# Kernel tuning notes

Measured on AMD Instinct MI355X. Metric: run time of the kernel, lower is better.

The kernel has to match this reference:

```python
import jax, jax.numpy as jnp
import numpy as np

N, D, H, F, T = 2048, 256, 4, 64, 64
HF = H * F


def setup_inputs() -> dict:
    key = jax.random.key(0)
    ks = jax.random.split(key, 24)
    f32 = jnp.float32
    emb = jax.random.normal(ks[0], (N, D), f32)
    y_as_x = jax.random.normal(ks[1], (N, T), f32)
    adj = (jax.random.uniform(ks[2], (N, N)) < 0.02).astype(f32)
    u = lambda k, shape, s: jax.random.uniform(k, shape, f32, -s, s)
    stdv = 1.0 / np.sqrt(HF)
    inp = dict(emb=emb, y_as_x=y_as_x, adj=adj)
    for i, p in enumerate(['pos', 'neg']):
        o = 3 + i * 6
        inp[p + '_w'] = u(ks[o], (D, HF), stdv)
        inp[p + '_wu'] = u(ks[o + 1], (H, F), 1.0)
        inp[p + '_wv'] = u(ks[o + 2], (H, F), 1.0)
        inp[p + '_b'] = u(ks[o + 3], (1, HF), stdv)
        inp[p + '_pw'] = u(ks[o + 4], (D, HF), 0.02)
        inp[p + '_pb'] = jnp.zeros((HF,), f32)
    inp['self_w'] = u(ks[15], (D, D), 0.02)
    inp['self_b'] = jnp.zeros((D,), f32)
    inp['mlp_pos_w'] = u(ks[16], (HF, D), 0.02)
    inp['mlp_pos_b'] = jnp.zeros((D,), f32)
    inp['mlp_neg_w'] = u(ks[17], (HF, D), 0.02)
    inp['mlp_neg_b'] = jnp.zeros((D,), f32)
    inp['sem_w1'] = u(ks[18], (D, D), 0.02)
    inp['sem_b1'] = jnp.zeros((D,), f32)
    inp['sem_w2'] = u(ks[19], (D, 1), 0.02)
    return inp


def _gat(x, mask, w, wu, wv, b, pw, pb):
    # x: [N,D], mask: [N,N] bool; multi-head GAT with dense masked softmax
    s = (x @ w).reshape(N, H, F).transpose(1, 0, 2)          # [H,N,F]
    f1 = jnp.einsum('hnf,hf->hn', s, wu)                     # u-score per node
    f2 = jnp.einsum('hnf,hf->hn', s, wv)                     # v-score per node
    logits = f1[:, None, :] + f2[:, :, None]                 # [H,N,N], i<-j
    logits = jax.nn.leaky_relu(logits, 0.2)
    masked = jnp.where(mask[None], logits, -1e9)
    attn = jnp.where(mask[None], jax.nn.softmax(masked, axis=2), 0.0)
    out = jnp.einsum('hij,hjf->hif', attn, s)                # [H,N,F]
    out = out.transpose(1, 0, 2).reshape(N, HF) + b
    return out + x @ pw + pb


def reference(emb, y_as_x, adj, pos_w, pos_wu, pos_wv, pos_b, pos_pw, pos_pb,
              neg_w, neg_wu, neg_wv, neg_b, neg_pw, neg_pb,
              self_w, self_b, mlp_pos_w, mlp_pos_b, mlp_neg_w, mlp_neg_b,
              sem_w1, sem_b1, sem_w2):
    # batched pairwise correlation (replaces the per-node Python loop)
    yc = y_as_x - y_as_x.mean(axis=1, keepdims=True)         # centered
    dot = yc @ yc.T                                          # [N,N]
    std = jnp.sqrt((yc ** 2).sum(axis=1) / (T - 1))          # torch std: ddof=1
    corr = dot / (std[:, None] * std[None, :])
    edge = adj != 0
    pos_mask = edge & (corr >= 0.1)
    neg_mask = edge & (corr < 0.1)

    pos_sup = _gat(emb, pos_mask, pos_w, pos_wu, pos_wv, pos_b, pos_pw, pos_pb)
    neg_sup = _gat(emb, neg_mask, neg_w, neg_wu, neg_wv, neg_b, neg_pw, neg_pb)

    sup = emb @ self_w + self_b
    pos_sup = pos_sup @ mlp_pos_w + mlp_pos_b
    neg_sup = neg_sup @ mlp_neg_w + mlp_neg_b

    all_emb = jnp.stack((sup, pos_sup, neg_sup), axis=1)     # [N,3,D]
    # semantic attention over the 3 relation channels
    wlog = jnp.tanh(all_emb @ sem_w1 + sem_b1) @ sem_w2      # [N,3,1]
    beta = jax.nn.softmax(wlog, axis=1)
    x = (beta * all_emb).sum(axis=1)                         # [N,D]
    # PairNorm PN-SI
    x = x - x.mean(axis=0)
    rownorm = jnp.sqrt(1e-6 + (x ** 2).sum(axis=1, keepdims=True))
    return x / rownorm
```

## Files before the change

kernel.cpp:

```cpp
#include <hip/hip_runtime.h>
#include <hip/hip_bf16.h>

#define KN  2048
#define KD  256
#define KH  4
#define KF  64
#define KT  64
#define NCS 32

typedef __attribute__((ext_vector_type(8))) short short8;
typedef __attribute__((ext_vector_type(4))) float floatx4;

__device__ __forceinline__ float wave_sum(float v) {
    #pragma unroll
    for (int o = 32; o > 0; o >>= 1) v += __shfl_xor(v, o, 64);
    return v;
}
__device__ __forceinline__ float wave_max(float v) {
    #pragma unroll
    for (int o = 32; o > 0; o >>= 1) v = fmaxf(v, __shfl_xor(v, o, 64));
    return v;
}
__device__ __forceinline__ short f2bs(float x) {
    union { __hip_bfloat16 h; short s; } u;
    u.h = __float2bfloat16(x);
    return u.s;
}

__global__ __launch_bounds__(256) void setup_kernel(const float* __restrict__ y,
                                                    float* __restrict__ ycs) {
    int w = threadIdx.x >> 6, lane = threadIdx.x & 63;
    int n = blockIdx.x * 4 + w;
    float v = y[n * KT + lane];
    float mean = wave_sum(v) * (1.0f / KT);
    float yc = v - mean;
    float ss = wave_sum(yc * yc);
    ycs[n * KT + lane] = yc * rsqrtf(ss * (1.0f / (KT - 1)));
}

__device__ __forceinline__ void corr_body(const float* __restrict__ ycs,
                                          const float* __restrict__ adj,
                                          unsigned char* __restrict__ code,
                                          int blk, char* smem) {
    float (*As)[68] = (float(*)[68])smem;
    float (*Bs)[68] = (float(*)[68])(smem + 4352);
    int bi = 0, rem = blk;
    while (rem >= 32 - bi) { rem -= 32 - bi; bi++; }
    int bj = bi + rem;
    int i0 = bi * 64, j0 = bj * 64;
    int t = threadIdx.x;
    int tx = t & 15, ty = t >> 4;
    int ar = t >> 2, ac = (t & 3) * 4;
    float acc[4][4] = {};
    for (int kt = 0; kt < KT; kt += 16) {
        float4 a4 = *reinterpret_cast<const float4*>(&ycs[(size_t)(i0 + ar) * KT + kt + ac]);
        float4 b4 = *reinterpret_cast<const float4*>(&ycs[(size_t)(j0 + ar) * KT + kt + ac]);
        As[ac + 0][ar] = a4.x; As[ac + 1][ar] = a4.y; As[ac + 2][ar] = a4.z; As[ac + 3][ar] = a4.w;
        Bs[ac + 0][ar] = b4.x; Bs[ac + 1][ar] = b4.y; Bs[ac + 2][ar] = b4.z; Bs[ac + 3][ar] = b4.w;
        __syncthreads();
        #pragma unroll
        for (int kk = 0; kk < 16; kk++) {
            float4 av = *reinterpret_cast<const float4*>(&As[kk][ty * 4]);
            float4 bv = *reinterpret_cast<const float4*>(&Bs[kk][tx * 4]);
            float a4v[4] = {av.x, av.y, av.z, av.w};
            float b4v[4] = {bv.x, bv.y, bv.z, bv.w};
            #pragma unroll
            for (int ii = 0; ii < 4; ii++)
                #pragma unroll
                for (int jj = 0; jj < 4; jj++) acc[ii][jj] += a4v[ii] * b4v[jj];
        }
        __syncthreads();
    }
    #pragma unroll
    for (int ii = 0; ii < 4; ii++) {
        int i = i0 + ty * 4 + ii;
        int jb = j0 + tx * 4;
        float4 av4 = *reinterpret_cast<const float4*>(&adj[(size_t)i * KN + jb]);
        float a4v[4] = {av4.x, av4.y, av4.z, av4.w};
        uchar4 cc;
        unsigned char* c = (unsigned char*)&cc;
        #pragma unroll
        for (int jj = 0; jj < 4; jj++)
            c[jj] = (a4v[jj] != 0.0f) ? ((acc[ii][jj] >= 0.1f) ? 1 : 2) : 0;
        *reinterpret_cast<uchar4*>(&code[(size_t)i * KN + jb]) = cc;
    }
    if (bi != bj) {
        #pragma unroll
        for (int jj = 0; jj < 4; jj++) {
            int j = j0 + tx * 4 + jj;
            int ib = i0 + ty * 4;
            float4 av4 = *reinterpret_cast<const float4*>(&adj[(size_t)j * KN + ib]);
            float a4v[4] = {av4.x, av4.y, av4.z, av4.w};
            uchar4 cc;
            unsigned char* c = (unsigned char*)&cc;
            #pragma unroll
            for (int ii = 0; ii < 4; ii++)
                c[ii] = (a4v[ii] != 0.0f) ? ((acc[ii][jj] >= 0.1f) ? 1 : 2) : 0;
            *reinterpret_cast<uchar4*>(&code[(size_t)j * KN + ib]) = cc;
        }
    }
}

template <bool TANH>
__device__ __forceinline__ void mfma_gemm_body(
    const float* __restrict__ A, int lda, int bm,
    const float* __restrict__ B, int ldb, int bn,
    const float* __restrict__ bias,
    float* __restrict__ C, int ldc, int cn,
    float* __restrict__ f1h, float* __restrict__ f2h,
    const float* __restrict__ wu_h, const float* __restrict__ wv_h,
    char* smem)
{
    short* As = (short*)smem;
    short* Bs = (short*)(smem + 5120);
    int t = threadIdx.x;
    int w = t >> 6, lane = t & 63;
    int m16 = lane & 15, kq = lane >> 4;
    floatx4 acc0 = {0,0,0,0}, acc1 = {0,0,0,0}, acc2 = {0,0,0,0}, acc3 = {0,0,0,0};
    int ar = t >> 2, acq = (t & 3) * 8;
    int bnn = t & 63, bkg = (t >> 6) * 8;
    for (int kt = 0; kt < KD; kt += 32) {
        const float* pa = &A[(size_t)(bm + ar) * lda + kt + acq];
        float4 a0 = *(const float4*)pa;
        float4 a1 = *(const float4*)(pa + 4);
        short8 av;
        av[0] = f2bs(a0.x); av[1] = f2bs(a0.y); av[2] = f2bs(a0.z); av[3] = f2bs(a0.w);
        av[4] = f2bs(a1.x); av[5] = f2bs(a1.y); av[6] = f2bs(a1.z); av[7] = f2bs(a1.w);
        const float* pb = &B[(size_t)(kt + bkg) * ldb + bn + bnn];
        short8 bv;
        #pragma unroll
        for (int u = 0; u < 8; u++) bv[u] = f2bs(pb[(size_t)u * ldb]);
        __syncthreads();
        *(short8*)&As[ar * 40 + acq] = av;
        *(short8*)&Bs[bnn * 40 + bkg] = bv;
        __syncthreads();
        short8 af  = *(short8*)&As[(w * 16 + m16) * 40 + kq * 8];
        short8 bf0 = *(short8*)&Bs[( 0 + m16) * 40 + kq * 8];
        short8 bf1 = *(short8*)&Bs[(16 + m16) * 40 + kq * 8];
        short8 bf2 = *(short8*)&Bs[(32 + m16) * 40 + kq * 8];
        short8 bf3 = *(short8*)&Bs[(48 + m16) * 40 + kq * 8];
        acc0 = __builtin_amdgcn_mfma_f32_16x16x32_bf16(af, bf0, acc0, 0, 0, 0);
        acc1 = __builtin_amdgcn_mfma_f32_16x16x32_bf16(af, bf1, acc1, 0, 0, 0);
        acc2 = __builtin_amdgcn_mfma_f32_16x16x32_bf16(af, bf2, acc2, 0, 0, 0);
        acc3 = __builtin_amdgcn_mfma_f32_16x16x32_bf16(af, bf3, acc3, 0, 0, 0);
    }
    int row0 = bm + w * 16 + kq * 4;
    floatx4 accs[4] = {acc0, acc1, acc2, acc3};
    #pragma unroll
    for (int nb = 0; nb < 4; nb++) {
        #pragma unroll
        for (int r = 0; r < 4; r++) {
            int col = nb * 16 + m16;
            float v = accs[nb][r] + (bias ? bias[col] : 0.0f);
            if (TANH) {
                float vc = fminf(fmaxf(v, -9.0f), 9.0f);
                float ex = __expf(2.0f * vc);
                v = (ex - 1.0f) / (ex + 1.0f);
            }
            C[(size_t)(row0 + r) * ldc + cn + col] = v;
        }
    }
    if (f1h) {
        float wuv[4], wvv[4];
        #pragma unroll
        for (int nb = 0; nb < 4; nb++) { wuv[nb] = wu_h[nb * 16 + m16]; wvv[nb] = wv_h[nb * 16 + m16]; }
        #pragma unroll
        for (int r = 0; r < 4; r++) {
            float p1 = accs[0][r] * wuv[0] + accs[1][r] * wuv[1] + accs[2][r] * wuv[2] + accs[3][r] * wuv[3];
            float p2 = accs[0][r] * wvv[0] + accs[1][r] * wvv[1] + accs[2][r] * wvv[2] + accs[3][r] * wvv[3];
            #pragma unroll
            for (int o = 1; o < 16; o <<= 1) {
                p1 += __shfl_xor(p1, o, 64);
                p2 += __shfl_xor(p2, o, 64);
            }
            if (m16 == 0) { f1h[row0 + r] = p1; f2h[row0 + r] = p2; }
        }
    }
}

struct EmbPtrs {
    float *S_pos, *S_neg, *P_pos, *P_neg, *sup;
    float *f1p, *f2p, *f1n, *f2n;
};
__global__ __launch_bounds__(256, 4) void phase1_kernel(
    const float* __restrict__ ycs, const float* __restrict__ adj,
    unsigned char* __restrict__ code,
    const float* __restrict__ emb,
    const float* __restrict__ pos_w, const float* __restrict__ neg_w,
    const float* __restrict__ pos_pw, const float* __restrict__ neg_pw,
    const float* __restrict__ self_w,
    const float* __restrict__ pos_pb, const float* __restrict__ neg_pb,
    const float* __restrict__ self_b,
    const float* __restrict__ pos_wu, const float* __restrict__ pos_wv,
    const float* __restrict__ neg_wu, const float* __restrict__ neg_wv,
    float* __restrict__ colsum, EmbPtrs ep)
{
    __shared__ alignas(16) char smem[10240];
    int blk = blockIdx.x;
    if (blk < 528) {
        corr_body(ycs, adj, code, blk, smem);
        return;
    }
    if (blk >= 1168) {
        for (int j = threadIdx.x; j < NCS * KD; j += 256) colsum[j] = 0.0f;
        return;
    }
    int b = blk - 528;
    int tn = b % 20, tm = b / 20;
    int buf = tn >> 2, coloff = (tn & 3) * 64;
    int h = tn & 3;
    const float* B; const float* bias; float* C;
    float *f1h = nullptr, *f2h = nullptr;
    const float *wu_h = nullptr, *wv_h = nullptr;
    if (buf == 0) {
        B = pos_w;  bias = nullptr; C = ep.S_pos;
        f1h = ep.f1p + h * KN; f2h = ep.f2p + h * KN;
        wu_h = pos_wu + h * KF; wv_h = pos_wv + h * KF;
    } else if (buf == 1) {
        B = neg_w;  bias = nullptr; C = ep.S_neg;
        f1h = ep.f1n + h * KN; f2h = ep.f2n + h * KN;
        wu_h = neg_wu + h * KF; wv_h = neg_wv + h * KF;
    } else if (buf == 2) { B = pos_pw; bias = pos_pb + coloff;  C = ep.P_pos; }
    else if (buf == 3)   { B = neg_pw; bias = neg_pb + coloff;  C = ep.P_neg; }
    else                 { B = self_w; bias = self_b + coloff;  C = ep.sup; }
    mfma_gemm_body<false>(emb, KD, tm * 64, B, KD, coloff, bias,
                          C, KD, coloff, f1h, f2h, wu_h, wv_h, smem);
}

__global__ __launch_bounds__(256, 4) void gemm_mlp(const float* __restrict__ Astack,
                                                   const float* __restrict__ B0,
                                                   const float* __restrict__ B1,
                                                   const float* __restrict__ b0,
                                                   const float* __restrict__ b1,
                                                   float* __restrict__ Cstack,
                                                   const float* __restrict__ sup,
                                                   const float* __restrict__ semw1,
                                                   const float* __restrict__ semb1,
                                                   float* __restrict__ T0) {
    __shared__ alignas(16) char smem[10240];
    int by = blockIdx.y;
    int cn = blockIdx.x * 64;
    if (by < 64) {
        int bm = by * 64;
        bool sel = bm >= KN;
        mfma_gemm_body<false>(Astack, KD, bm, sel ? B1 : B0, KD, cn,
                              (sel ? b1 : b0) + cn, Cstack, KD, cn,
                              nullptr, nullptr, nullptr, nullptr, smem);
    } else {
        int bm = (by - 64) * 64;
        mfma_gemm_body<true>(sup, KD, bm, semw1, KD, cn,
                             semb1 + cn, T0, KD, cn,
                             nullptr, nullptr, nullptr, nullptr, smem);
    }
}

__global__ __launch_bounds__(256, 4) void gemm_sem(const float* __restrict__ Astack,
                                                   const float* __restrict__ B,
                                                   const float* __restrict__ bias,
                                                   float* __restrict__ Cstack) {
    __shared__ alignas(16) char smem[10240];
    int cn = blockIdx.x * 64;
    mfma_gemm_body<true>(Astack, KD, blockIdx.y * 64, B, KD, cn,
                         bias + cn, Cstack, KD, cn,
                         nullptr, nullptr, nullptr, nullptr, smem);
}

#define MAXE 256
__global__ __launch_bounds__(256) void attn_kernel(
    const unsigned char* __restrict__ code,
    const float* __restrict__ f1p, const float* __restrict__ f2p,
    const float* __restrict__ Sp, const float* __restrict__ Pp,
    const float* __restrict__ bp, float* __restrict__ Gp,
    const float* __restrict__ f1n, const float* __restrict__ f2n,
    const float* __restrict__ Sn, const float* __restrict__ Pn,
    const float* __restrict__ bn_, float* __restrict__ Gn)
{
    __shared__ alignas(16) int jl[MAXE];
    __shared__ alignas(16) float lg[KH][MAXE];
    __shared__ int cnt;
    int blk = blockIdx.x;
    int rel = blk >> 11;
    int i = blk & (KN - 1);
    unsigned char want = rel ? (unsigned char)2 : (unsigned char)1;
    const float* f1 = rel ? f1n : f1p;
    const float* f2 = rel ? f2n : f2p;
    const float* S  = rel ? Sn : Sp;
    const float* P  = rel ? Pn : Pp;
    const float* b  = rel ? bn_ : bp;
    float* G        = rel ? Gn : Gp;
    int w = threadIdx.x >> 6, lane = threadIdx.x & 63;
    if (threadIdx.x == 0) cnt = 0;
    __syncthreads();
    #pragma unroll
    for (int it = 0; it < 2; it++) {
        int base = w * 512 + it * 256;
        uchar4 cv = *reinterpret_cast<const uchar4*>(&code[(size_t)i * KN + base + lane * 4]);
        const unsigned char* ce = (const unsigned char*)&cv;
        #pragma unroll
        for (int e = 0; e < 4; e++) {
            bool p = (ce[e] == want);
            unsigned long long bal = __ballot(p);
            int tot = __popcll(bal);
            int basepos = 0;
            if (lane == 0 && tot) basepos = atomicAdd(&cnt, tot);
            basepos = __shfl(basepos, 0, 64);
            if (p) {
                int idx = basepos + __popcll(bal & ((1ull << lane) - 1ull));
                if (idx < MAXE) jl[idx] = base + lane * 4 + e;
            }
        }
    }
    __syncthreads();
    int count = cnt; if (count > MAXE) count = MAXE;
    int countR = (count + 3) & ~3;
    if (threadIdx.x < countR - count) jl[count + threadIdx.x] = 0;
    __syncthreads();
    int h = w;
    float f2i = f2[h * KN + i];
    float m = -1e30f;
    for (int k = lane; k < count; k += 64) {
        int j = jl[k];
        float x = f1[h * KN + j] + f2i;
        x = (x > 0.0f) ? x : 0.2f * x;
        lg[h][k] = x;
        m = fmaxf(m, x);
    }
    m = wave_max(m);
    float ps = 0.0f;
    for (int k = lane; k < count; k += 64) {
        float e = __expf(lg[h][k] - m);
        lg[h][k] = e;
        ps += e;
    }
    float denom = wave_sum(ps);
    for (int k2 = count + lane; k2 < countR; k2 += 64) lg[h][k2] = 0.0f;
    int g = lane >> 4, q4 = (lane & 15) * 4;
    const float* Sh4 = S + h * KF + q4;
    float ax = 0.0f, ay = 0.0f, az = 0.0f, aw = 0.0f;
    for (int k = 0; k < countR; k += 4) {
        int j = jl[k + g];
        float wgt = lg[h][k + g];
        float4 sv = *reinterpret_cast<const float4*>(&Sh4[(size_t)j * KD]);
        ax += wgt * sv.x; ay += wgt * sv.y; az += wgt * sv.z; aw += wgt * sv.w;
    }
    #pragma unroll
    for (int o = 16; o < 64; o <<= 1) {
        ax += __shfl_xor(ax, o, 64); ay += __shfl_xor(ay, o, 64);
        az += __shfl_xor(az, o, 64); aw += __shfl_xor(aw, o, 64);
    }
    if (g == 0) {
        float inv = count ? (1.0f / denom) : 0.0f;
        int col = h * KF + q4;
        size_t idx = (size_t)i * KD + col;
        float4 pv = *reinterpret_cast<const float4*>(&P[idx]);
        float4 o4;
        o4.x = ax * inv + b[col + 0] + pv.x;
        o4.y = ay * inv + b[col + 1] + pv.y;
        o4.z = az * inv + b[col + 2] + pv.z;
        o4.w = aw * inv + b[col + 3] + pv.w;
        *reinterpret_cast<float4*>(&G[idx]) = o4;
    }
}

__global__ __launch_bounds__(256) void combine_kernel(const float* __restrict__ T0,
                                                      const float* __restrict__ T1,
                                                      const float* __restrict__ T2,
                                                      const float* __restrict__ w2,
                                                      const float* __restrict__ sup,
                                                      const float* __restrict__ psup,
                                                      const float* __restrict__ nsup,
                                                      float* __restrict__ X,
                                                      float* __restrict__ colsum) {
    int n = blockIdx.x, d = threadIdx.x;
    size_t idx = (size_t)n * KD + d;
    float w2d = w2[d];
    float p0 = T0[idx] * w2d, p1 = T1[idx] * w2d, p2 = T2[idx] * w2d;
    __shared__ float sbuf[4][3];
    int wv = d >> 6, lane = d & 63;
    float s0 = wave_sum(p0), s1 = wave_sum(p1), s2 = wave_sum(p2);
    if (lane == 0) { sbuf[wv][0] = s0; sbuf[wv][1] = s1; sbuf[wv][2] = s2; }
    __syncthreads();
    float w0 = sbuf[0][0] + sbuf[1][0] + sbuf[2][0] + sbuf[3][0];
    float w1 = sbuf[0][1] + sbuf[1][1] + sbuf[2][1] + sbuf[3][1];
    float w2l = sbuf[0][2] + sbuf[1][2] + sbuf[2][2] + sbuf[3][2];
    float mm = fmaxf(w0, fmaxf(w1, w2l));
    float e0 = __expf(w0 - mm), e1 = __expf(w1 - mm), e2 = __expf(w2l - mm);
    float inv = 1.0f / (e0 + e1 + e2);
    float x = (e0 * inv) * sup[idx] + (e1 * inv) * psup[idx] + (e2 * inv) * nsup[idx];
    X[idx] = x;
    atomicAdd(&colsum[(n & (NCS - 1)) * KD + d], x);
}

__global__ __launch_bounds__(256) void final_kernel(const float* __restrict__ X,
                                                    const float* __restrict__ colsum,
                                                    float* __restrict__ out) {
    int n = blockIdx.x, d = threadIdx.x;
    float cs = 0.0f;
    #pragma unroll
    for (int r = 0; r < NCS; r++) cs += colsum[r * KD + d];
    float mean = cs * (1.0f / KN);
    float xc = X[(size_t)n * KD + d] - mean;
    __shared__ float sbuf[4];
    int wv = d >> 6, lane = d & 63;
    float s = wave_sum(xc * xc);
    if (lane == 0) sbuf[wv] = s;
    __syncthreads();
    float ss = sbuf[0] + sbuf[1] + sbuf[2] + sbuf[3];
    out[(size_t)n * KD + d] = xc * rsqrtf(1e-6f + ss);
}

extern "C" void kernel_launch(void* const* d_in, const int* in_sizes, int n_in,
                              void* d_out, int out_size, void* d_ws, size_t ws_size,
                              hipStream_t stream) {
    typedef const float* fp;
    fp emb    = (fp)d_in[0];
    fp y_as_x = (fp)d_in[1];
    fp adj    = (fp)d_in[2];
    fp pos_w  = (fp)d_in[3],  pos_wu = (fp)d_in[4],  pos_wv = (fp)d_in[5];
    fp pos_b  = (fp)d_in[6],  pos_pw = (fp)d_in[7],  pos_pb = (fp)d_in[8];
    fp neg_w  = (fp)d_in[9],  neg_wu = (fp)d_in[10], neg_wv = (fp)d_in[11];
    fp neg_b  = (fp)d_in[12], neg_pw = (fp)d_in[13], neg_pb = (fp)d_in[14];
    fp self_w = (fp)d_in[15], self_b = (fp)d_in[16];
    fp mlp_pos_w = (fp)d_in[17], mlp_pos_b = (fp)d_in[18];
    fp mlp_neg_w = (fp)d_in[19], mlp_neg_b = (fp)d_in[20];
    fp sem_w1 = (fp)d_in[21], sem_b1 = (fp)d_in[22], sem_w2 = (fp)d_in[23];
    float* out = (float*)d_out;

    char* ws = (char*)d_ws;
    float* ycs        = (float*)(ws + 0x0000000);
    unsigned char* cd = (unsigned char*)(ws + 0x0080000);
    float* S_pos      = (float*)(ws + 0x0480000);
    float* S_neg      = (float*)(ws + 0x0680000);
    float* P_pos      = (float*)(ws + 0x0880000);
    float* P_neg      = (float*)(ws + 0x0A80000);
    float* G_pos      = (float*)(ws + 0x0C80000);
    float* G_neg      = (float*)(ws + 0x0E80000);
    float* sup        = (float*)(ws + 0x1080000);
    float* psup       = (float*)(ws + 0x1280000);
    float* nsup       = (float*)(ws + 0x1480000);
    float* colsum     = (float*)(ws + 0x1680000);
    float* f1p        = (float*)(ws + 0x1700000);
    float* f2p        = (float*)(ws + 0x1708000);
    float* f1n        = (float*)(ws + 0x1710000);
    float* f2n        = (float*)(ws + 0x1718000);
    float* T0 = P_pos, *T1 = P_neg, *T2 = G_pos, *X = G_neg;

    setup_kernel<<<512, 256, 0, stream>>>(y_as_x, ycs);

    EmbPtrs ep = {S_pos, S_neg, P_pos, P_neg, sup, f1p, f2p, f1n, f2n};
    phase1_kernel<<<528 + 640 + 1, 256, 0, stream>>>(ycs, adj, cd, emb,
                                                     pos_w, neg_w, pos_pw, neg_pw, self_w,
                                                     pos_pb, neg_pb, self_b,
                                                     pos_wu, pos_wv, neg_wu, neg_wv,
                                                     colsum, ep);

    attn_kernel<<<2 * KN, 256, 0, stream>>>(cd,
                                            f1p, f2p, S_pos, P_pos, pos_b, G_pos,
                                            f1n, f2n, S_neg, P_neg, neg_b, G_neg);

    gemm_mlp<<<dim3(4, 96), 256, 0, stream>>>(G_pos, mlp_pos_w, mlp_neg_w,
                                              mlp_pos_b, mlp_neg_b, psup,
                                              sup, sem_w1, sem_b1, T0);
    gemm_sem<<<dim3(4, 64), 256, 0, stream>>>(psup, sem_w1, sem_b1, T1);

    combine_kernel<<<KN, 256, 0, stream>>>(T0, T1, T2, sem_w2, sup, psup, nsup, X, colsum);
    final_kernel<<<KN, 256, 0, stream>>>(X, colsum, out);
}
```

Before: 170.3 us.

## Pre-convert weights and activations to transposed bf16 and merge attention relations

A setup stage now converts emb to bf16 and transposes all eight weight matrices into bf16 ahead of time. The GEMM bodies can then load contiguous short8 vectors instead of doing strided fp32 loads and converting on every tile. Intermediate activations (G, sup, psup) are also written as bf16 for the later GEMMs to consume. The attention kernel now handles both relations in one block per node, scanning the adjacency code row once instead of twice. The cost is extra workspace, extra conversion blocks in setup, and bf16 rounding of some intermediates.

```diff
diff --git a/kernel.cpp b/kernel.cpp
--- a/kernel.cpp
+++ b/kernel.cpp
@@ -9,6 +9,7 @@
 #define NCS 32
 
 typedef __attribute__((ext_vector_type(8))) short short8;
+typedef __attribute__((ext_vector_type(4))) short short4v;
 typedef __attribute__((ext_vector_type(4))) float floatx4;
 
 __device__ __forceinline__ float wave_sum(float v) {
@@ -27,15 +28,56 @@
     return u.s;
 }
 
+struct CvtPtrs {
+    const float* emb; short* emb_bf;
+    const float* src[8];
+    short* dst[8];
+};
 __global__ __launch_bounds__(256) void setup_kernel(const float* __restrict__ y,
-                                                    float* __restrict__ ycs) {
-    int w = threadIdx.x >> 6, lane = threadIdx.x & 63;
-    int n = blockIdx.x * 4 + w;
-    float v = y[n * KT + lane];
-    float mean = wave_sum(v) * (1.0f / KT);
-    float yc = v - mean;
-    float ss = wave_sum(yc * yc);
-    ycs[n * KT + lane] = yc * rsqrtf(ss * (1.0f / (KT - 1)));
+                                                    float* __restrict__ ycs,
+                                                    CvtPtrs cp) {
+    __shared__ float tl[64][65];
+    int blk = blockIdx.x;
+    int t = threadIdx.x;
+    if (blk < 512) {
+        int w = t >> 6, lane = t & 63;
+        int n = blk * 4 + w;
+        float v = y[n * KT + lane];
+        float mean = wave_sum(v) * (1.0f / KT);
+        float yc = v - mean;
+        float ss = wave_sum(yc * yc);
+        ycs[n * KT + lane] = yc * rsqrtf(ss * (1.0f / (KT - 1)));
+        return;
+    }
+    if (blk < 768) {
+        int base = (blk - 512) * 2048 + t * 8;
+        float4 a = *reinterpret_cast<const float4*>(&cp.emb[base]);
+        float4 b = *reinterpret_cast<const float4*>(&cp.emb[base + 4]);
+        short8 v;
+        v[0] = f2bs(a.x); v[1] = f2bs(a.y); v[2] = f2bs(a.z); v[3] = f2bs(a.w);
+        v[4] = f2bs(b.x); v[5] = f2bs(b.y); v[6] = f2bs(b.z); v[7] = f2bs(b.w);
+        *reinterpret_cast<short8*>(&cp.emb_bf[base]) = v;
+        return;
+    }
+    int b = blk - 768;
+    int m = b >> 4, tile = b & 15;
+    int ti = tile >> 2, tj = tile & 3;
+    const float* W = cp.src[m];
+    short* WT = cp.dst[m];
+    int n = t & 63, kg = (t >> 6) * 16;
+    #pragma unroll
+    for (int r2 = 0; r2 < 16; r2++)
+        tl[n][kg + r2] = W[(size_t)(ti * 64 + kg + r2) * KD + tj * 64 + n];
+    __syncthreads();
+    int nr = t >> 2, kc = (t & 3) * 16;
+    short8 v0, v1;
+    #pragma unroll
+    for (int c = 0; c < 8; c++) v0[c] = f2bs(tl[nr][kc + c]);
+    #pragma unroll
+    for (int c = 0; c < 8; c++) v1[c] = f2bs(tl[nr][kc + 8 + c]);
+    size_t o = (size_t)(tj * 64 + nr) * KD + ti * 64 + kc;
+    *reinterpret_cast<short8*>(&WT[o]) = v0;
+    *reinterpret_cast<short8*>(&WT[o + 8]) = v1;
 }
 
 __device__ __forceinline__ void corr_body(const float* __restrict__ ycs,
@@ -103,10 +145,11 @@
 
 template <bool TANH>
 __device__ __forceinline__ void mfma_gemm_body(
-    const float* __restrict__ A, int lda, int bm,
-    const float* __restrict__ B, int ldb, int bn,
+    const short* __restrict__ A, int bm,
+    const short* __restrict__ BT, int bn,
     const float* __restrict__ bias,
-    float* __restrict__ C, int ldc, int cn,
+    float* __restrict__ C, int cn,
+    short* __restrict__ Cbf,
     float* __restrict__ f1h, float* __restrict__ f2h,
     const float* __restrict__ wu_h, const float* __restrict__ wv_h,
     char* smem)
@@ -117,28 +160,21 @@
     int w = t >> 6, lane = t & 63;
     int m16 = lane & 15, kq = lane >> 4;
     floatx4 acc0 = {0,0,0,0}, acc1 = {0,0,0,0}, acc2 = {0,0,0,0}, acc3 = {0,0,0,0};
-    int ar = t >> 2, acq = (t & 3) * 8;
-    int bnn = t & 63, bkg = (t >> 6) * 8;
+    int r = t >> 2, ko = (t & 3) * 8;
+    const short* pa = &A[(size_t)(bm + r) * KD + ko];
+    const short* pb = &BT[(size_t)(bn + r) * KD + ko];
     for (int kt = 0; kt < KD; kt += 32) {
-        const float* pa = &A[(size_t)(bm + ar) * lda + kt + acq];
-        float4 a0 = *(const float4*)pa;
-        float4 a1 = *(const float4*)(pa + 4);
-        short8 av;
-        av[0] = f2bs(a0.x); av[1] = f2bs(a0.y); av[2] = f2bs(a0.z); av[3] = f2bs(a0.w);
-        av[4] = f2bs(a1.x); av[5] = f2bs(a1.y); av[6] = f2bs(a1.z); av[7] = f2bs(a1.w);
-        const float* pb = &B[(size_t)(kt + bkg) * ldb + bn + bnn];
-        short8 bv;
-        #pragma unroll
-        for (int u = 0; u < 8; u++) bv[u] = f2bs(pb[(size_t)u * ldb]);
+        short8 av = *reinterpret_cast<const short8*>(pa + kt);
+        short8 bv = *reinterpret_cast<const short8*>(pb + kt);
         __syncthreads();
-        *(short8*)&As[ar * 40 + acq] = av;
-        *(short8*)&Bs[bnn * 40 + bkg] = bv;
+        *reinterpret_cast<short8*>(&As[r * 40 + ko]) = av;
+        *reinterpret_cast<short8*>(&Bs[r * 40 + ko]) = bv;
         __syncthreads();
-        short8 af  = *(short8*)&As[(w * 16 + m16) * 40 + kq * 8];
-        short8 bf0 = *(short8*)&Bs[( 0 + m16) * 40 + kq * 8];
-        short8 bf1 = *(short8*)&Bs[(16 + m16) * 40 + kq * 8];
-        short8 bf2 = *(short8*)&Bs[(32 + m16) * 40 + kq * 8];
-        short8 bf3 = *(short8*)&Bs[(48 + m16) * 40 + kq * 8];
+        short8 af  = *reinterpret_cast<short8*>(&As[(w * 16 + m16) * 40 + kq * 8]);
+        short8 bf0 = *reinterpret_cast<short8*>(&Bs[( 0 + m16) * 40 + kq * 8]);
+        short8 bf1 = *reinterpret_cast<short8*>(&Bs[(16 + m16) * 40 + kq * 8]);
+        short8 bf2 = *reinterpret_cast<short8*>(&Bs[(32 + m16) * 40 + kq * 8]);
+        short8 bf3 = *reinterpret_cast<short8*>(&Bs[(48 + m16) * 40 + kq * 8]);
         acc0 = __builtin_amdgcn_mfma_f32_16x16x32_bf16(af, bf0, acc0, 0, 0, 0);
         acc1 = __builtin_amdgcn_mfma_f32_16x16x32_bf16(af, bf1, acc1, 0, 0, 0);
         acc2 = __builtin_amdgcn_mfma_f32_16x16x32_bf16(af, bf2, acc2, 0, 0, 0);
@@ -149,15 +185,17 @@
     #pragma unroll
     for (int nb = 0; nb < 4; nb++) {
         #pragma unroll
-        for (int r = 0; r < 4; r++) {
+        for (int rr = 0; rr < 4; rr++) {
             int col = nb * 16 + m16;
-            float v = accs[nb][r] + (bias ? bias[col] : 0.0f);
+            float v = accs[nb][rr] + (bias ? bias[col] : 0.0f);
             if (TANH) {
                 float vc = fminf(fmaxf(v, -9.0f), 9.0f);
                 float ex = __expf(2.0f * vc);
                 v = (ex - 1.0f) / (ex + 1.0f);
             }
-            C[(size_t)(row0 + r) * ldc + cn + col] = v;
+            size_t cidx = (size_t)(row0 + rr) * KD + cn + col;
+            C[cidx] = v;
+            if (Cbf) Cbf[cidx] = f2bs(v);
         }
     }
     if (f1h) {
@@ -165,35 +203,30 @@
         #pragma unroll
         for (int nb = 0; nb < 4; nb++) { wuv[nb] = wu_h[nb * 16 + m16]; wvv[nb] = wv_h[nb * 16 + m16]; }
         #pragma unroll
-        for (int r = 0; r < 4; r++) {
-            float p1 = accs[0][r] * wuv[0] + accs[1][r] * wuv[1] + accs[2][r] * wuv[2] + accs[3][r] * wuv[3];
-            float p2 = accs[0][r] * wvv[0] + accs[1][r] * wvv[1] + accs[2][r] * wvv[2] + accs[3][r] * wvv[3];
+        for (int rr = 0; rr < 4; rr++) {
+            float p1 = accs[0][rr] * wuv[0] + accs[1][rr] * wuv[1] + accs[2][rr] * wuv[2] + accs[3][rr] * wuv[3];
+            float p2 = accs[0][rr] * wvv[0] + accs[1][rr] * wvv[1] + accs[2][rr] * wvv[2] + accs[3][rr] * wvv[3];
             #pragma unroll
             for (int o = 1; o < 16; o <<= 1) {
                 p1 += __shfl_xor(p1, o, 64);
                 p2 += __shfl_xor(p2, o, 64);
             }
-            if (m16 == 0) { f1h[row0 + r] = p1; f2h[row0 + r] = p2; }
-        }
-    }
-}
-
-struct EmbPtrs {
+            if (m16 == 0) { f1h[row0 + rr] = p1; f2h[row0 + rr] = p2; }
+        }
+    }
+}
+
+struct P1Ptrs {
+    const short *emb_bf, *pos_wT, *neg_wT, *pos_pwT, *neg_pwT, *self_wT;
+    const float *pos_pb, *neg_pb, *self_b;
+    const float *pos_wu, *pos_wv, *neg_wu, *neg_wv;
     float *S_pos, *S_neg, *P_pos, *P_neg, *sup;
+    short *sup_bf;
     float *f1p, *f2p, *f1n, *f2n;
 };
 __global__ __launch_bounds__(256, 4) void phase1_kernel(
     const float* __restrict__ ycs, const float* __restrict__ adj,
-    unsigned char* __restrict__ code,
-    const float* __restrict__ emb,
-    const float* __restrict__ pos_w, const float* __restrict__ neg_w,
-    const float* __restrict__ pos_pw, const float* __restrict__ neg_pw,
-    const float* __restrict__ self_w,
-    const float* __restrict__ pos_pb, const float* __restrict__ neg_pb,
-    const float* __restrict__ self_b,
-    const float* __restrict__ pos_wu, const float* __restrict__ pos_wv,
-    const float* __restrict__ neg_wu, const float* __restrict__ neg_wv,
-    float* __restrict__ colsum, EmbPtrs ep)
+    unsigned char* __restrict__ code, float* __restrict__ colsum, P1Ptrs p)
 {
     __shared__ alignas(16) char smem[10240];
     int blk = blockIdx.x;
@@ -209,32 +242,141 @@
     int tn = b % 20, tm = b / 20;
     int buf = tn >> 2, coloff = (tn & 3) * 64;
     int h = tn & 3;
-    const float* B; const float* bias; float* C;
+    const short* B; const float* bias = nullptr; float* C; short* Cbf = nullptr;
     float *f1h = nullptr, *f2h = nullptr;
     const float *wu_h = nullptr, *wv_h = nullptr;
     if (buf == 0) {
-        B = pos_w;  bias = nullptr; C = ep.S_pos;
-        f1h = ep.f1p + h * KN; f2h = ep.f2p + h * KN;
-        wu_h = pos_wu + h * KF; wv_h = pos_wv + h * KF;
+        B = p.pos_wT;  C = p.S_pos;
+        f1h = p.f1p + h * KN; f2h = p.f2p + h * KN;
+        wu_h = p.pos_wu + h * KF; wv_h = p.pos_wv + h * KF;
     } else if (buf == 1) {
-        B = neg_w;  bias = nullptr; C = ep.S_neg;
-        f1h = ep.f1n + h * KN; f2h = ep.f2n + h * KN;
-        wu_h = neg_wu + h * KF; wv_h = neg_wv + h * KF;
-    } else if (buf == 2) { B = pos_pw; bias = pos_pb + coloff;  C = ep.P_pos; }
-    else if (buf == 3)   { B = neg_pw; bias = neg_pb + coloff;  C = ep.P_neg; }
-    else                 { B = self_w; bias = self_b + coloff;  C = ep.sup; }
-    mfma_gemm_body<false>(emb, KD, tm * 64, B, KD, coloff, bias,
-                          C, KD, coloff, f1h, f2h, wu_h, wv_h, smem);
-}
-
-__global__ __launch_bounds__(256, 4) void gemm_mlp(const float* __restrict__ Astack,
-                                                   const float* __restrict__ B0,
-                                                   const float* __restrict__ B1,
+        B = p.neg_wT;  C = p.S_neg;
+        f1h = p.f1n + h * KN; f2h = p.f2n + h * KN;
+        wu_h = p.neg_wu + h * KF; wv_h = p.neg_wv + h * KF;
+    } else if (buf == 2) { B = p.pos_pwT; bias = p.pos_pb + coloff; C = p.P_pos; }
+    else if (buf == 3)   { B = p.neg_pwT; bias = p.neg_pb + coloff; C = p.P_neg; }
+    else                 { B = p.self_wT; bias = p.self_b + coloff; C = p.sup; Cbf = p.sup_bf; }
+    mfma_gemm_body<false>(p.emb_bf, tm * 64, B, coloff, bias,
+                          C, coloff, Cbf, f1h, f2h, wu_h, wv_h, smem);
+}
+
+#define MAXE 256
+__global__ __launch_bounds__(256) void attn_kernel(
+    const unsigned char* __restrict__ code,
+    const float* __restrict__ f1p, const float* __restrict__ f2p,
+    const float* __restrict__ Sp, const float* __restrict__ Pp,
+    const float* __restrict__ bp, short* __restrict__ Gp,
+    const float* __restrict__ f1n, const float* __restrict__ f2n,
+    const float* __restrict__ Sn, const float* __restrict__ Pn,
+    const float* __restrict__ bn_, short* __restrict__ Gn)
+{
+    __shared__ alignas(16) int jl[2][MAXE];
+    __shared__ alignas(16) float lg[KH][MAXE];
+    __shared__ int cnt[2];
+    int i = blockIdx.x;
+    int w = threadIdx.x >> 6, lane = threadIdx.x & 63;
+    if (threadIdx.x < 2) cnt[threadIdx.x] = 0;
+    __syncthreads();
+    #pragma unroll
+    for (int it = 0; it < 2; it++) {
+        int base = w * 512 + it * 256;
+        uchar4 cv = *reinterpret_cast<const uchar4*>(&code[(size_t)i * KN + base + lane * 4]);
+        const unsigned char* ce = (const unsigned char*)&cv;
+        #pragma unroll
+        for (int e = 0; e < 4; e++) {
+            #pragma unroll
+            for (int rel = 0; rel < 2; rel++) {
+                bool pr = (ce[e] == (rel ? (unsigned char)2 : (unsigned char)1));
+                unsigned long long bal = __ballot(pr);
+                int tot = __popcll(bal);
+                int basepos = 0;
+                if (lane == 0 && tot) basepos = atomicAdd(&cnt[rel], tot);
+                basepos = __shfl(basepos, 0, 64);
+                if (pr) {
+                    int idx = basepos + __popcll(bal & ((1ull << lane) - 1ull));
+                    if (idx < MAXE) jl[rel][idx] = base + lane * 4 + e;
+                }
+            }
+        }
+    }
+    __syncthreads();
+    int c0 = cnt[0]; if (c0 > MAXE) c0 = MAXE;
+    int c1 = cnt[1]; if (c1 > MAXE) c1 = MAXE;
+    if (threadIdx.x < 4) {
+        int cR = (c0 + 3) & ~3;
+        if (c0 + threadIdx.x < cR) jl[0][c0 + threadIdx.x] = 0;
+    } else if (threadIdx.x < 8) {
+        int l2 = threadIdx.x - 4;
+        int cR = (c1 + 3) & ~3;
+        if (c1 + l2 < cR) jl[1][c1 + l2] = 0;
+    }
+    __syncthreads();
+    int h = w;
+    int g = lane >> 4, q4 = (lane & 15) * 4;
+    for (int rel = 0; rel < 2; rel++) {
+        const float* f1 = rel ? f1n : f1p;
+        const float* f2 = rel ? f2n : f2p;
+        const float* S  = rel ? Sn : Sp;
+        const float* P  = rel ? Pn : Pp;
+        const float* b  = rel ? bn_ : bp;
+        short* G        = rel ? Gn : Gp;
+        int count = rel ? c1 : c0;
+        int countR = (count + 3) & ~3;
+        float f2i = f2[h * KN + i];
+        float m = -1e30f;
+        for (int k = lane; k < count; k += 64) {
+            int j = jl[rel][k];
+            float x = f1[h * KN + j] + f2i;
+            x = (x > 0.0f) ? x : 0.2f * x;
+            lg[h][k] = x;
+            m = fmaxf(m, x);
+        }
+        m = wave_max(m);
+        float ps = 0.0f;
+        for (int k = lane; k < count; k += 64) {
+            float e = __expf(lg[h][k] - m);
+            lg[h][k] = e;
+            ps += e;
+        }
+        float denom = wave_sum(ps);
+        for (int k2 = count + lane; k2 < countR; k2 += 64) lg[h][k2] = 0.0f;
+        const float* Sh4 = S + h * KF + q4;
+        float ax = 0.0f, ay = 0.0f, az = 0.0f, aw = 0.0f;
+        for (int k = 0; k < countR; k += 4) {
+            int j = jl[rel][k + g];
+            float wgt = lg[h][k + g];
+            float4 sv = *reinterpret_cast<const float4*>(&Sh4[(size_t)j * KD]);
+            ax += wgt * sv.x; ay += wgt * sv.y; az += wgt * sv.z; aw += wgt * sv.w;
+        }
+        #pragma unroll
+        for (int o = 16; o < 64; o <<= 1) {
+            ax += __shfl_xor(ax, o, 64); ay += __shfl_xor(ay, o, 64);
+            az += __shfl_xor(az, o, 64); aw += __shfl_xor(aw, o, 64);
+        }
+        if (g == 0) {
+            float inv = count ? (1.0f / denom) : 0.0f;
+            int col = h * KF + q4;
+            size_t idx = (size_t)i * KD + col;
+            float4 pv = *reinterpret_cast<const float4*>(&P[idx]);
+            short4v o4;
+            o4[0] = f2bs(ax * inv + b[col + 0] + pv.x);
+            o4[1] = f2bs(ay * inv + b[col + 1] + pv.y);
+            o4[2] = f2bs(az * inv + b[col + 2] + pv.z);
+            o4[3] = f2bs(aw * inv + b[col + 3] + pv.w);
+            *reinterpret_cast<short4v*>(&G[idx]) = o4;
+        }
+    }
+}
+
+__global__ __launch_bounds__(256, 4) void gemm_mlp(const short* __restrict__ Astack,
+                                                   const short* __restrict__ B0T,
+                                                   const short* __restrict__ B1T,
                                                    const float* __restrict__ b0,
                                                    const float* __restrict__ b1,
                                                    float* __restrict__ Cstack,
-                                                   const float* __restrict__ sup,
-                                                   const float* __restrict__ semw1,
+                                                   short* __restrict__ Cstack_bf,
+                                                   const short* __restrict__ sup_bf,
+                                                   const short* __restrict__ semw1T,
                                                    const float* __restrict__ semb1,
                                                    float* __restrict__ T0) {
     __shared__ alignas(16) char smem[10240];
@@ -243,123 +385,26 @@
     if (by < 64) {
         int bm = by * 64;
         bool sel = bm >= KN;
-        mfma_gemm_body<false>(Astack, KD, bm, sel ? B1 : B0, KD, cn,
-                              (sel ? b1 : b0) + cn, Cstack, KD, cn,
+        mfma_gemm_body<false>(Astack, bm, sel ? B1T : B0T, cn,
+                              (sel ? b1 : b0) + cn, Cstack, cn, Cstack_bf,
                               nullptr, nullptr, nullptr, nullptr, smem);
     } else {
         int bm = (by - 64) * 64;
-        mfma_gemm_body<true>(sup, KD, bm, semw1, KD, cn,
-                             semb1 + cn, T0, KD, cn,
+        mfma_gemm_body<true>(sup_bf, bm, semw1T, cn,
+                             semb1 + cn, T0, cn, nullptr,
                              nullptr, nullptr, nullptr, nullptr, smem);
     }
 }
 
-__global__ __launch_bounds__(256, 4) void gemm_sem(const float* __restrict__ Astack,
-                                                   const float* __restrict__ B,
+__global__ __launch_bounds__(256, 4) void gemm_sem(const short* __restrict__ Astack,
+                                                   const short* __restrict__ BT,
                                                    const float* __restrict__ bias,
                                                    float* __restrict__ Cstack) {
     __shared__ alignas(16) char smem[10240];
     int cn = blockIdx.x * 64;
-    mfma_gemm_body<true>(Astack, KD, blockIdx.y * 64, B, KD, cn,
-                         bias + cn, Cstack, KD, cn,
+    mfma_gemm_body<true>(Astack, blockIdx.y * 64, BT, cn,
+                         bias + cn, Cstack, cn, nullptr,
                          nullptr, nullptr, nullptr, nullptr, smem);
-}
-
-#define MAXE 256
-__global__ __launch_bounds__(256) void attn_kernel(
-    const unsigned char* __restrict__ code,
-    const float* __restrict__ f1p, const float* __restrict__ f2p,
-    const float* __restrict__ Sp, const float* __restrict__ Pp,
-    const float* __restrict__ bp, float* __restrict__ Gp,
-    const float* __restrict__ f1n, const float* __restrict__ f2n,
-    const float* __restrict__ Sn, const float* __restrict__ Pn,
-    const float* __restrict__ bn_, float* __restrict__ Gn)
-{
-    __shared__ alignas(16) int jl[MAXE];
-    __shared__ alignas(16) float lg[KH][MAXE];
-    __shared__ int cnt;
-    int blk = blockIdx.x;
-    int rel = blk >> 11;
-    int i = blk & (KN - 1);
-    unsigned char want = rel ? (unsigned char)2 : (unsigned char)1;
-    const float* f1 = rel ? f1n : f1p;
-    const float* f2 = rel ? f2n : f2p;
-    const float* S  = rel ? Sn : Sp;
-    const float* P  = rel ? Pn : Pp;
-    const float* b  = rel ? bn_ : bp;
-    float* G        = rel ? Gn : Gp;
-    int w = threadIdx.x >> 6, lane = threadIdx.x & 63;
-    if (threadIdx.x == 0) cnt = 0;
-    __syncthreads();
-    #pragma unroll
-    for (int it = 0; it < 2; it++) {
-        int base = w * 512 + it * 256;
-        uchar4 cv = *reinterpret_cast<const uchar4*>(&code[(size_t)i * KN + base + lane * 4]);
-        const unsigned char* ce = (const unsigned char*)&cv;
-        #pragma unroll
-        for (int e = 0; e < 4; e++) {
-            bool p = (ce[e] == want);
-            unsigned long long bal = __ballot(p);
-            int tot = __popcll(bal);
-            int basepos = 0;
-            if (lane == 0 && tot) basepos = atomicAdd(&cnt, tot);
-            basepos = __shfl(basepos, 0, 64);
-            if (p) {
-                int idx = basepos + __popcll(bal & ((1ull << lane) - 1ull));
-                if (idx < MAXE) jl[idx] = base + lane * 4 + e;
-            }
-        }
-    }
-    __syncthreads();
-    int count = cnt; if (count > MAXE) count = MAXE;
-    int countR = (count + 3) & ~3;
-    if (threadIdx.x < countR - count) jl[count + threadIdx.x] = 0;
-    __syncthreads();
-    int h = w;
-    float f2i = f2[h * KN + i];
-    float m = -1e30f;
-    for (int k = lane; k < count; k += 64) {
-        int j = jl[k];
-        float x = f1[h * KN + j] + f2i;
-        x = (x > 0.0f) ? x : 0.2f * x;
-        lg[h][k] = x;
-        m = fmaxf(m, x);
-    }
-    m = wave_max(m);
-    float ps = 0.0f;
-    for (int k = lane; k < count; k += 64) {
-        float e = __expf(lg[h][k] - m);
-        lg[h][k] = e;
-        ps += e;
-    }
-    float denom = wave_sum(ps);
-    for (int k2 = count + lane; k2 < countR; k2 += 64) lg[h][k2] = 0.0f;
-    int g = lane >> 4, q4 = (lane & 15) * 4;
-    const float* Sh4 = S + h * KF + q4;
-    float ax = 0.0f, ay = 0.0f, az = 0.0f, aw = 0.0f;
-    for (int k = 0; k < countR; k += 4) {
-        int j = jl[k + g];
-        float wgt = lg[h][k + g];
-        float4 sv = *reinterpret_cast<const float4*>(&Sh4[(size_t)j * KD]);
-        ax += wgt * sv.x; ay += wgt * sv.y; az += wgt * sv.z; aw += wgt * sv.w;
-    }
-    #pragma unroll
-    for (int o = 16; o < 64; o <<= 1) {
-        ax += __shfl_xor(ax, o, 64); ay += __shfl_xor(ay, o, 64);
-        az += __shfl_xor(az, o, 64); aw += __shfl_xor(aw, o, 64);
-    }
-    if (g == 0) {
-        float inv = count ? (1.0f / denom) : 0.0f;
-        int col = h * KF + q4;
-        size_t idx = (size_t)i * KD + col;
-        float4 pv = *reinterpret_cast<const float4*>(&P[idx]);
-        float4 o4;
-        o4.x = ax * inv + b[col + 0] + pv.x;
-        o4.y = ay * inv + b[col + 1] + pv.y;
-        o4.z = az * inv + b[col + 2] + pv.z;
-        o4.w = aw * inv + b[col + 3] + pv.w;
-        *reinterpret_cast<float4*>(&G[idx]) = o4;
-    }
 }
 
 __global__ __launch_bounds__(256) void combine_kernel(const float* __restrict__ T0,
@@ -427,41 +472,82 @@
     float* out = (float*)d_out;
 
     char* ws = (char*)d_ws;
-    float* ycs        = (float*)(ws + 0x0000000);
-    unsigned char* cd = (unsigned char*)(ws + 0x0080000);
-    float* S_pos      = (float*)(ws + 0x0480000);
-    float* S_neg      = (float*)(ws + 0x0680000);
-    float* P_pos      = (float*)(ws + 0x0880000);
-    float* P_neg      = (float*)(ws + 0x0A80000);
-    float* G_pos      = (float*)(ws + 0x0C80000);
-    float* G_neg      = (float*)(ws + 0x0E80000);
-    float* sup        = (float*)(ws + 0x1080000);
-    float* psup       = (float*)(ws + 0x1280000);
-    float* nsup       = (float*)(ws + 0x1480000);
-    float* colsum     = (float*)(ws + 0x1680000);
-    float* f1p        = (float*)(ws + 0x1700000);
-    float* f2p        = (float*)(ws + 0x1708000);
-    float* f1n        = (float*)(ws + 0x1710000);
-    float* f2n        = (float*)(ws + 0x1718000);
-    float* T0 = P_pos, *T1 = P_neg, *T2 = G_pos, *X = G_neg;
-
-    setup_kernel<<<512, 256, 0, stream>>>(y_as_x, ycs);
-
-    EmbPtrs ep = {S_pos, S_neg, P_pos, P_neg, sup, f1p, f2p, f1n, f2n};
-    phase1_kernel<<<528 + 640 + 1, 256, 0, stream>>>(ycs, adj, cd, emb,
-                                                     pos_w, neg_w, pos_pw, neg_pw, self_w,
-                                                     pos_pb, neg_pb, self_b,
-                                                     pos_wu, pos_wv, neg_wu, neg_wv,
-                                                     colsum, ep);
-
-    attn_kernel<<<2 * KN, 256, 0, stream>>>(cd,
-                                            f1p, f2p, S_pos, P_pos, pos_b, G_pos,
-                                            f1n, f2n, S_neg, P_neg, neg_b, G_neg);
-
-    gemm_mlp<<<dim3(4, 96), 256, 0, stream>>>(G_pos, mlp_pos_w, mlp_neg_w,
-                                              mlp_pos_b, mlp_neg_b, psup,
-                                              sup, sem_w1, sem_b1, T0);
-    gemm_sem<<<dim3(4, 64), 256, 0, stream>>>(psup, sem_w1, sem_b1, T1);
+    size_t off = 0;
+    auto alloc = [&](size_t sz) -> char* {
+        char* p = ws + off;
+        off += (sz + 511) & ~(size_t)511;
+        return p;
+    };
+    const size_t MAT_F32 = (size_t)KN * KD * 4;
+    const size_t MAT_BF  = (size_t)KN * KD * 2;
+    const size_t W_BF    = (size_t)KD * KD * 2;
+
+    float* ycs         = (float*)alloc((size_t)KN * KT * 4);
+    unsigned char* cd  = (unsigned char*)alloc((size_t)KN * KN);
+    float* S_pos       = (float*)alloc(MAT_F32);
+    float* S_neg       = (float*)alloc(MAT_F32);
+    float* P_pos       = (float*)alloc(MAT_F32);
+    float* P_neg       = (float*)alloc(MAT_F32);
+    float* sup         = (float*)alloc(MAT_F32);
+    float* psup        = (float*)alloc(2 * MAT_F32);
+    float* nsup        = psup + (size_t)KN * KD;
+    float* T0          = (float*)alloc(MAT_F32);
+    float* T1          = (float*)alloc(2 * MAT_F32);
+    float* T2          = T1 + (size_t)KN * KD;
+    float* X           = (float*)alloc(MAT_F32);
+    float* colsum      = (float*)alloc((size_t)NCS * KD * 4);
+    float* f1p         = (float*)alloc((size_t)KH * KN * 4);
+    float* f2p         = (float*)alloc((size_t)KH * KN * 4);
+    float* f1n         = (float*)alloc((size_t)KH * KN * 4);
+    float* f2n         = (float*)alloc((size_t)KH * KN * 4);
+    short* emb_bf      = (short*)alloc(MAT_BF);
+    short* G_bf        = (short*)alloc(2 * MAT_BF);
+    short* Gp_bf       = G_bf;
+    short* Gn_bf       = G_bf + (size_t)KN * KD;
+    short* sup_bf      = (short*)alloc(MAT_BF);
+    short* ps_bf       = (short*)alloc(2 * MAT_BF);
+    short* pos_wT      = (short*)alloc(W_BF);
+    short* neg_wT      = (short*)alloc(W_BF);
+    short* pos_pwT     = (short*)alloc(W_BF);
+    short* neg_pwT     = (short*)alloc(W_BF);
+    short* self_wT     = (short*)alloc(W_BF);
+    short* mlp_posT    = (short*)alloc(W_BF);
+    short* mlp_negT    = (short*)alloc(W_BF);
+    short* semw1T      = (short*)alloc(W_BF);
+
+    CvtPtrs cp;
+    cp.emb = emb; cp.emb_bf = emb_bf;
+    cp.src[0] = pos_w;     cp.dst[0] = pos_wT;
+    cp.src[1] = neg_w;     cp.dst[1] = neg_wT;
+    cp.src[2] = pos_pw;    cp.dst[2] = pos_pwT;
+    cp.src[3] = neg_pw;    cp.dst[3] = neg_pwT;
+    cp.src[4] = self_w;    cp.dst[4] = self_wT;
+    cp.src[5] = mlp_pos_w; cp.dst[5] = mlp_posT;
+    cp.src[6] = mlp_neg_w; cp.dst[6] = mlp_negT;
+    cp.src[7] = sem_w1;    cp.dst[7] = semw1T;
+
+    setup_kernel<<<512 + 256 + 128, 256, 0, stream>>>(y_as_x, ycs, cp);
+
+    P1Ptrs p1;
+    p1.emb_bf = emb_bf;
+    p1.pos_wT = pos_wT; p1.neg_wT = neg_wT;
+    p1.pos_pwT = pos_pwT; p1.neg_pwT = neg_pwT; p1.self_wT = self_wT;
+    p1.pos_pb = pos_pb; p1.neg_pb = neg_pb; p1.self_b = self_b;
+    p1.pos_wu = pos_wu; p1.pos_wv = pos_wv; p1.neg_wu = neg_wu; p1.neg_wv = neg_wv;
+    p1.S_pos = S_pos; p1.S_neg = S_neg; p1.P_pos = P_pos; p1.P_neg = P_neg;
+    p1.sup = sup; p1.sup_bf = sup_bf;
+    p1.f1p = f1p; p1.f2p = f2p; p1.f1n = f1n; p1.f2n = f2n;
+
+    phase1_kernel<<<528 + 640 + 1, 256, 0, stream>>>(ycs, adj, cd, colsum, p1);
+
+    attn_kernel<<<KN, 256, 0, stream>>>(cd,
+                                        f1p, f2p, S_pos, P_pos, pos_b, Gp_bf,
+                                        f1n, f2n, S_neg, P_neg, neg_b, Gn_bf);
+
+    gemm_mlp<<<dim3(4, 96), 256, 0, stream>>>(G_bf, mlp_posT, mlp_negT,
+                                              mlp_pos_b, mlp_neg_b, psup, ps_bf,
+                                              sup_bf, semw1T, sem_b1, T0);
+    gemm_sem<<<dim3(4, 64), 256, 0, stream>>>(ps_bf, semw1T, sem_b1, T1);
 
     combine_kernel<<<KN, 256, 0, stream>>>(T0, T1, T2, sem_w2, sup, psup, nsup, X, colsum);
     final_kernel<<<KN, 256, 0, stream>>>(X, colsum, out);
```

Result: no change. 170.1 us (-0.1%).
